# Kernel tuning notes

Measured on AMD Instinct MI355X. Metric: run time of the kernel, lower is better.

The kernel has to match this reference:

```python
import jax, jax.numpy as jnp
import numpy as np

B, S, D = 4, 2048, 1024
H, DK, DV = 16, 64, 64


def setup_inputs() -> dict:
    key = jax.random.key(0)
    ks = jax.random.split(key, 12)
    scale = 1.0 / np.sqrt(D)
    queries = jax.random.normal(ks[0], (B, S, D), dtype=jnp.float32)
    keys_ = jax.random.normal(ks[1], (B, S, D), dtype=jnp.float32)
    values = jax.random.normal(ks[2], (B, S, D), dtype=jnp.float32)
    # binary additive mask (1 = masked out), broadcastable over batch and heads
    mask = jax.random.randint(ks[3], (1, 1, S, S), 0, 2).astype(jnp.float32)
    Wq = jax.random.normal(ks[4], (D, H * DK), dtype=jnp.float32) * scale
    bq = jnp.zeros((H * DK,), dtype=jnp.float32)
    Wk = jax.random.normal(ks[5], (D, H * DK), dtype=jnp.float32) * scale
    bk = jnp.zeros((H * DK,), dtype=jnp.float32)
    Wv = jax.random.normal(ks[6], (D, H * DV), dtype=jnp.float32) * scale
    bv = jnp.zeros((H * DV,), dtype=jnp.float32)
    Wo = jax.random.normal(ks[7], (H * DV, D), dtype=jnp.float32) * scale
    bo = jnp.zeros((D,), dtype=jnp.float32)
    return {"queries": queries, "keys": keys_, "values": values, "mask": mask,
            "Wq": Wq, "bq": bq, "Wk": Wk, "bk": bk, "Wv": Wv, "bv": bv,
            "Wo": Wo, "bo": bo}


def reference(queries, keys, values, mask, Wq, bq, Wk, bk, Wv, bv, Wo, bo):
    b = queries.shape[0]
    # projections + split heads: [B, S, H*Dh] -> [B, H, S, Dh]
    q = (queries @ Wq + bq).reshape(b, -1, H, DK).transpose(0, 2, 1, 3)
    k = (keys @ Wk + bk).reshape(b, -1, H, DK).transpose(0, 2, 1, 3)
    v = (values @ Wv + bv).reshape(b, -1, H, DV).transpose(0, 2, 1, 3)
    scores = jnp.einsum("bhqd,bhkd->bhqk", q, k) / jnp.sqrt(jnp.float32(DK))
    scores = scores + mask * (-1e9)
    attn = jax.nn.softmax(scores, axis=-1)
    ctx = jnp.einsum("bhqk,bhkd->bhqd", attn, v)  # [B, H, S, DV]
    ctx = ctx.transpose(0, 2, 1, 3).reshape(b, -1, H * DV)
    return ctx @ Wo + bo
```

## Files before the change

### kernel.cpp

```cpp
#include <hip/hip_runtime.h>
#include <cstdint>
#include <cstddef>

typedef __attribute__((ext_vector_type(8))) short bf16x8;
typedef __attribute__((ext_vector_type(4))) short bf16x4;
typedef __attribute__((ext_vector_type(4))) float f32x4;

__device__ __forceinline__ unsigned short f2bf(float f) {
    union { float f; unsigned int u; } v; v.f = f;
    unsigned int r = v.u + 0x7FFFu + ((v.u >> 16) & 1u);
    return (unsigned short)(r >> 16);
}
__device__ __forceinline__ unsigned int pk2(float a, float b) {
    return (unsigned int)f2bf(a) | ((unsigned int)f2bf(b) << 16);
}
__device__ __forceinline__ unsigned int pkpair(float a, float b) {
#if __has_builtin(__builtin_amdgcn_cvt_pk_bf16_f32)
    auto r = __builtin_amdgcn_cvt_pk_bf16_f32(a, b);
    return __builtin_bit_cast(unsigned int, r);
#else
    unsigned int ua = __builtin_bit_cast(unsigned int, a) + 0x8000u;
    unsigned int ub = __builtin_bit_cast(unsigned int, b) + 0x8000u;
    return __builtin_amdgcn_perm(ub, ua, 0x07060302u);
#endif
}

typedef __attribute__((address_space(1))) void gvoid;
typedef __attribute__((address_space(3))) void svoid;
__device__ __forceinline__ void ld16_lds(const void* g, void* l) {
    __builtin_amdgcn_global_load_lds((gvoid*)g, (svoid*)l, 16, 0, 0);
}

#define QSCALE 0.1803368801111204f

__global__ __launch_bounds__(256)
void preprocess(const float* __restrict__ Qin, const float* __restrict__ Kin,
                const float* __restrict__ Vin, const float* __restrict__ Msk,
                const float* __restrict__ Wq, const float* __restrict__ Wk,
                const float* __restrict__ Wv, const float* __restrict__ Wo,
                unsigned short* __restrict__ acts, unsigned char* __restrict__ mbits,
                unsigned short* __restrict__ wts)
{
    __shared__ float t[32][33];
    const int bx = blockIdx.x, tid = threadIdx.x;
    if (bx < 12288) {
        const int which = bx >> 12;
        const float* src = (which == 0) ? Qin : (which == 1) ? Kin : Vin;
        unsigned short* dst = acts + ((size_t)which << 23);
        const size_t i = ((size_t)(bx & 4095) * 256 + tid) * 8;
        float4 a = *(const float4*)(src + i);
        float4 b = *(const float4*)(src + i + 4);
        uint4 p;
        p.x = pk2(a.x, a.y); p.y = pk2(a.z, a.w);
        p.z = pk2(b.x, b.y); p.w = pk2(b.z, b.w);
        *(uint4*)(dst + i) = p;
    } else if (bx < 14336) {
        const size_t i = ((size_t)(bx - 12288) * 256 + tid) * 8;
        float4 a = *(const float4*)(Msk + i);
        float4 b = *(const float4*)(Msk + i + 4);
        unsigned c = 0;
        c |= (a.x != 0.f) ? 1u : 0u;
        c |= (a.y != 0.f) ? 2u : 0u;
        c |= (a.z != 0.f) ? 4u : 0u;
        c |= (a.w != 0.f) ? 8u : 0u;
        c |= (b.x != 0.f) ? 16u : 0u;
        c |= (b.y != 0.f) ? 32u : 0u;
        c |= (b.z != 0.f) ? 64u : 0u;
        c |= (b.w != 0.f) ? 128u : 0u;
        mbits[i >> 3] = (unsigned char)c;
    } else {
        const int idx = bx - 14336;
        const int z = idx >> 10, rem = idx & 1023;
        const float* W = (z == 0) ? Wq : (z == 1) ? Wk : (z == 2) ? Wv : Wo;
        unsigned short* Wt = wts + ((size_t)z << 20);
        const int n0 = (rem & 31) << 5, k0 = (rem >> 5) << 5;
        const int tx = tid & 31, ty = tid >> 5;
#pragma unroll
        for (int i = 0; i < 4; i++)
            t[ty + 8 * i][tx] = W[(size_t)(k0 + ty + 8 * i) * 1024 + n0 + tx];
        __syncthreads();
#pragma unroll
        for (int i = 0; i < 4; i++)
            Wt[(size_t)(n0 + ty + 8 * i) * 1024 + k0 + tx] = f2bf(t[tx][ty + 8 * i]);
    }
}

__global__ __launch_bounds__(256, 4)
void qkv_gemm(const unsigned short* __restrict__ A0,
              const unsigned short* __restrict__ W0,
              const float* __restrict__ bq, const float* __restrict__ bk,
              const float* __restrict__ bv,
              unsigned short* __restrict__ out0)
{
    __shared__ __align__(16) unsigned short sm[18432];

    const int z = blockIdx.z;
    const unsigned short* A  = A0 + ((size_t)z << 23);
    const unsigned short* Wt = W0 + ((size_t)z << 20);
    const float* bias = (z == 0) ? bq : (z == 1) ? bk : bv;
    unsigned short* ob = out0 + ((size_t)z << 23);

    const int tid = threadIdx.x, lane = tid & 63, wave = tid >> 6;
    const int quad = lane >> 4, l16 = lane & 15;
    const int wr = wave >> 1, wc = wave & 1;
    const int m0 = blockIdx.x * 128, n0 = blockIdx.y * 128;

    const char* Ab = (const char*)A  + (size_t)m0 * 2048;
    const char* Bb = (const char*)Wt + (size_t)n0 * 2048;
    const int sr0 = tid >> 2, sc0 = (tid & 3) << 4;

    f32x4 acc[4][4];
#pragma unroll
    for (int i = 0; i < 4; i++)
#pragma unroll
        for (int j = 0; j < 4; j++) acc[i][j] = (f32x4){0.f, 0.f, 0.f, 0.f};

    {
        char* Ad = (char*)sm;
        char* Bd = Ad + 8192;
        ld16_lds(Ab + (size_t)sr0 * 2048 + sc0,        Ad + tid * 16);
        ld16_lds(Ab + (size_t)(sr0 + 64) * 2048 + sc0, Ad + (256 + tid) * 16);
        ld16_lds(Bb + (size_t)sr0 * 2048 + sc0,        Bd + tid * 16);
        ld16_lds(Bb + (size_t)(sr0 + 64) * 2048 + sc0, Bd + (256 + tid) * 16);
    }

    for (int it = 0; it < 32; ++it) {
        const int cur = it & 1;
        __syncthreads();
        if (it < 31) {
            const int kb2 = (it + 1) * 64;
            char* Ad = (char*)(sm + (cur ^ 1) * 8192);
            char* Bd = Ad + 8192;
            ld16_lds(Ab + (size_t)sr0 * 2048 + kb2 + sc0,        Ad + tid * 16);
            ld16_lds(Ab + (size_t)(sr0 + 64) * 2048 + kb2 + sc0, Ad + (256 + tid) * 16);
            ld16_lds(Bb + (size_t)sr0 * 2048 + kb2 + sc0,        Bd + tid * 16);
            ld16_lds(Bb + (size_t)(sr0 + 64) * 2048 + kb2 + sc0, Bd + (256 + tid) * 16);
        }
        const unsigned short* As = sm + cur * 8192;
        const unsigned short* Bs = As + 4096;

        bf16x8 af[4], bfr[4];
#pragma unroll
        for (int mt = 0; mt < 4; mt++)
            af[mt] = *(const bf16x8*)&As[(wr * 64 + mt * 16 + l16) * 32 + quad * 8];
#pragma unroll
        for (int nt = 0; nt < 4; nt++)
            bfr[nt] = *(const bf16x8*)&Bs[(wc * 64 + nt * 16 + l16) * 32 + quad * 8];
#pragma unroll
        for (int mt = 0; mt < 4; mt++)
#pragma unroll
            for (int nt = 0; nt < 4; nt++)
                acc[mt][nt] = __builtin_amdgcn_mfma_f32_16x16x32_bf16(af[mt], bfr[nt], acc[mt][nt], 0, 0, 0);
    }

    float bvv[4];
#pragma unroll
    for (int nt = 0; nt < 4; nt++) bvv[nt] = bias[n0 + wc * 64 + nt * 16 + l16];

    if (z < 2) {
#pragma unroll
        for (int mt = 0; mt < 4; mt++) {
            const int m = m0 + wr * 64 + mt * 16 + quad * 4;
            const int b = m >> 11;
#pragma unroll
            for (int nt = 0; nt < 4; nt++) {
                const int n = n0 + wc * 64 + nt * 16 + l16;
                const int h = n >> 6, dk = n & 63;
#pragma unroll
                for (int r = 0; r < 4; r++) {
                    const int s = (m + r) & 2047;
                    float o = acc[mt][nt][r] + bvv[nt];
                    if (z == 0) o *= QSCALE;
                    ob[((size_t)((b << 4) + h) * 2048 + s) * 64 + dk] = f2bf(o);
                }
            }
        }
    } else {
        __syncthreads();
        unsigned short* T = sm + wave * (64 * 72);
#pragma unroll
        for (int mt = 0; mt < 4; mt++)
#pragma unroll
            for (int nt = 0; nt < 4; nt++)
#pragma unroll
                for (int r = 0; r < 4; r++)
                    T[(nt * 16 + l16) * 72 + mt * 16 + quad * 4 + r] = f2bf(acc[mt][nt][r] + bvv[nt]);
        __syncthreads();
#pragma unroll
        for (int i = 0; i < 8; i++) {
            const int nl = i * 8 + (lane >> 3);
            const int mc = lane & 7;
            uint4 v = *(const uint4*)&T[nl * 72 + mc * 8];
            const int n  = n0 + wc * 64 + nl;
            const int mg = m0 + wr * 64 + mc * 8;
            const int b = mg >> 11, s = mg & 2047;
            const int h = n >> 6, dv = n & 63;
            *(uint4*)&ob[((size_t)((b << 4) + h) * 64 + dv) * 2048 + s] = v;
        }
    }
}

__global__ __launch_bounds__(256, 3)
void gemm_final(const unsigned short* __restrict__ A,
                const unsigned short* __restrict__ Wt, const float* __restrict__ bias,
                float* __restrict__ of)
{
    __shared__ __align__(16) unsigned short sm[16384];

    const int tid = threadIdx.x, lane = tid & 63, wave = tid >> 6;
    const int quad = lane >> 4, l16 = lane & 15;
    const int wr = wave >> 1, wc = wave & 1;
    const int m0 = blockIdx.x * 128, n0 = blockIdx.y * 128;

    const char* Ab = (const char*)A  + (size_t)m0 * 2048;
    const char* Bb = (const char*)Wt + (size_t)n0 * 2048;
    const int sr0 = tid >> 2, sc0 = (tid & 3) << 4;

    f32x4 acc[4][4];
#pragma unroll
    for (int i = 0; i < 4; i++)
#pragma unroll
        for (int j = 0; j < 4; j++) acc[i][j] = (f32x4){0.f, 0.f, 0.f, 0.f};

    {
        char* Ad = (char*)sm;
        char* Bd = Ad + 8192;
        ld16_lds(Ab + (size_t)sr0 * 2048 + sc0,        Ad + tid * 16);
        ld16_lds(Ab + (size_t)(sr0 + 64) * 2048 + sc0, Ad + (256 + tid) * 16);
        ld16_lds(Bb + (size_t)sr0 * 2048 + sc0,        Bd + tid * 16);
        ld16_lds(Bb + (size_t)(sr0 + 64) * 2048 + sc0, Bd + (256 + tid) * 16);
    }

    for (int it = 0; it < 32; ++it) {
        const int cur = it & 1;
        __syncthreads();
        if (it < 31) {
            const int kb2 = (it + 1) * 64;
            char* Ad = (char*)(sm + (cur ^ 1) * 8192);
            char* Bd = Ad + 8192;
            ld16_lds(Ab + (size_t)sr0 * 2048 + kb2 + sc0,        Ad + tid * 16);
            ld16_lds(Ab + (size_t)(sr0 + 64) * 2048 + kb2 + sc0, Ad + (256 + tid) * 16);
            ld16_lds(Bb + (size_t)sr0 * 2048 + kb2 + sc0,        Bd + tid * 16);
            ld16_lds(Bb + (size_t)(sr0 + 64) * 2048 + kb2 + sc0, Bd + (256 + tid) * 16);
        }
        const unsigned short* As = sm + cur * 8192;
        const unsigned short* Bs = As + 4096;

        bf16x8 af[4], bfr[4];
#pragma unroll
        for (int mt = 0; mt < 4; mt++)
            af[mt] = *(const bf16x8*)&As[(wr * 64 + mt * 16 + l16) * 32 + quad * 8];
#pragma unroll
        for (int nt = 0; nt < 4; nt++)
            bfr[nt] = *(const bf16x8*)&Bs[(wc * 64 + nt * 16 + l16) * 32 + quad * 8];
#pragma unroll
        for (int mt = 0; mt < 4; mt++)
#pragma unroll
            for (int nt = 0; nt < 4; nt++)
                acc[mt][nt] = __builtin_amdgcn_mfma_f32_16x16x32_bf16(af[mt], bfr[nt], acc[mt][nt], 0, 0, 0);
    }

    float bvv[4];
#pragma unroll
    for (int nt = 0; nt < 4; nt++) bvv[nt] = bias[n0 + wc * 64 + nt * 16 + l16];
#pragma unroll
    for (int mt = 0; mt < 4; mt++) {
        const int m = m0 + wr * 64 + mt * 16 + quad * 4;
#pragma unroll
        for (int nt = 0; nt < 4; nt++) {
            const int n = n0 + wc * 64 + nt * 16 + l16;
#pragma unroll
            for (int r = 0; r < 4; r++)
                of[(size_t)(m + r) * 1024 + n] = acc[mt][nt][r] + bvv[nt];
        }
    }
}

__global__ __launch_bounds__(256, 4)
void attn_kernel(const unsigned short* __restrict__ q,
                 const unsigned short* __restrict__ k,
                 const unsigned short* __restrict__ vT,
                 const unsigned int* __restrict__ mbits,
                 unsigned short* __restrict__ ctx)
{
    __shared__ __align__(16) unsigned short Ks[2][64 * 64];
    __shared__ __align__(16) unsigned short Vs[2][64 * 64];

    const int tid = threadIdx.x, lane = tid & 63, wave = tid >> 6;
    const int quad = lane >> 4, l16 = lane & 15;
    const int sw = l16 & 7;
    const int bid = blockIdx.x;
    const int qblk = bid & 15, h = (bid >> 4) & 15, b = bid >> 8;

    const unsigned short* qb = q  + (size_t)(b * 16 + h) * 2048 * 64;
    const unsigned short* kb = k  + (size_t)(b * 16 + h) * 2048 * 64;
    const unsigned short* vb = vT + (size_t)(b * 16 + h) * 64 * 2048;

    const int c0 = tid, c1 = 256 + tid;
    const int r0 = c0 >> 3, gcc0 = (c0 & 7) ^ (r0 & 7);
    const int r1 = c1 >> 3, gcc1 = (c1 & 7) ^ (r1 & 7);

    int qrow[2];
    bf16x8 qf[2][2];
    f32x4 O0[4], O1[4];
    f32x4 lacc0 = (f32x4){0.f,0.f,0.f,0.f}, lacc1 = (f32x4){0.f,0.f,0.f,0.f};
    const bf16x4 vones = (bf16x4){(short)0x3F80, (short)0x3F80, (short)0x3F80, (short)0x3F80};
#pragma unroll
    for (int g = 0; g < 2; g++) {
        qrow[g] = qblk * 128 + wave * 32 + g * 16 + l16;
        qf[g][0] = *(const bf16x8*)&qb[qrow[g] * 64 + quad * 8];
        qf[g][1] = *(const bf16x8*)&qb[qrow[g] * 64 + 32 + quad * 8];
    }
#pragma unroll
    for (int i = 0; i < 4; i++) { O0[i] = (f32x4){0.f,0.f,0.f,0.f}; O1[i] = (f32x4){0.f,0.f,0.f,0.f}; }
    const unsigned int* mrow0 = mbits + (size_t)qrow[0] * 64;
    const unsigned int* mrow1 = mbits + (size_t)qrow[1] * 64;

    {
        ld16_lds((const char*)kb + (size_t)r0 * 128 + gcc0 * 16, (char*)Ks[0] + c0 * 16);
        ld16_lds((const char*)kb + (size_t)r1 * 128 + gcc1 * 16, (char*)Ks[0] + c1 * 16);
        ld16_lds((const char*)vb + (size_t)r0 * 4096 + gcc0 * 16, (char*)Vs[0] + c0 * 16);
        ld16_lds((const char*)vb + (size_t)r1 * 4096 + gcc1 * 16, (char*)Vs[0] + c1 * 16);
    }
    uint2 mwc0 = *(const uint2*)&mrow0[0];
    uint2 mwc1 = *(const uint2*)&mrow1[0];

    for (int it = 0; it < 32; ++it) {
        const int kt = it << 6;
        const int cur = it & 1, nxt = cur ^ 1;
        __syncthreads();

        if (it < 31) {
            const char* kg = (const char*)kb + (size_t)(kt + 64) * 128;
            const char* vg = (const char*)vb + (size_t)(kt + 64) * 2;
            ld16_lds(kg + (size_t)r0 * 128 + gcc0 * 16, (char*)Ks[nxt] + c0 * 16);
            ld16_lds(kg + (size_t)r1 * 128 + gcc1 * 16, (char*)Ks[nxt] + c1 * 16);
            ld16_lds(vg + (size_t)r0 * 4096 + gcc0 * 16, (char*)Vs[nxt] + c0 * 16);
            ld16_lds(vg + (size_t)r1 * 4096 + gcc1 * 16, (char*)Vs[nxt] + c1 * 16);
        }
        const int mi = (it < 31) ? ((kt + 64) >> 5) : 0;
        uint2 mwn0 = *(const uint2*)&mrow0[mi];
        uint2 mwn1 = *(const uint2*)&mrow1[mi];

        const unsigned short* Kc = Ks[cur];
        const unsigned short* Vc = Vs[cur];

        f32x4 S0[4], S1[4];
        __builtin_amdgcn_s_setprio(1);
#pragma unroll
        for (int mt = 0; mt < 4; mt++) {
            const unsigned short* kp = Kc + (mt * 16 + l16) * 64;
            bf16x8 ka0 = *(const bf16x8*)&kp[((quad    ) ^ sw) * 8];
            bf16x8 ka1 = *(const bf16x8*)&kp[((4 + quad) ^ sw) * 8];
            f32x4 z0 = (f32x4){0.f,0.f,0.f,0.f};
            f32x4 z1 = (f32x4){0.f,0.f,0.f,0.f};
            z0 = __builtin_amdgcn_mfma_f32_16x16x32_bf16(ka0, qf[0][0], z0, 0, 0, 0);
            S0[mt] = __builtin_amdgcn_mfma_f32_16x16x32_bf16(ka1, qf[0][1], z0, 0, 0, 0);
            z1 = __builtin_amdgcn_mfma_f32_16x16x32_bf16(ka0, qf[1][0], z1, 0, 0, 0);
            S1[mt] = __builtin_amdgcn_mfma_f32_16x16x32_bf16(ka1, qf[1][1], z1, 0, 0, 0);
        }
        __builtin_amdgcn_s_setprio(0);
        bf16x4 pf0[4], pf1[4];
#pragma unroll
        for (int mt = 0; mt < 4; mt++) {
            const unsigned int wm0 = ((mt & 2) ? mwc0.y : mwc0.x) >> (((mt & 1) << 4) + (quad << 2));
            const unsigned int wm1 = ((mt & 2) ? mwc1.y : mwc1.x) >> (((mt & 1) << 4) + (quad << 2));
            float p0[4], p1[4];
#pragma unroll
            for (int r = 0; r < 4; r++) {
                p0[r] = __builtin_amdgcn_exp2f(((wm0 >> r) & 1u) ? -1e8f : S0[mt][r]);
                p1[r] = __builtin_amdgcn_exp2f(((wm1 >> r) & 1u) ? -1e8f : S1[mt][r]);
            }
            uint2 u0, u1;
            u0.x = pkpair(p0[0], p0[1]); u0.y = pkpair(p0[2], p0[3]);
            u1.x = pkpair(p1[0], p1[1]); u1.y = pkpair(p1[2], p1[3]);
            pf0[mt] = __builtin_bit_cast(bf16x4, u0);
            pf1[mt] = __builtin_bit_cast(bf16x4, u1);
        }
        __builtin_amdgcn_s_setprio(1);
#pragma unroll
        for (int mt = 0; mt < 4; mt++) {
            lacc0 = __builtin_amdgcn_mfma_f32_16x16x16bf16_1k(vones, pf0[mt], lacc0, 0, 0, 0);
            lacc1 = __builtin_amdgcn_mfma_f32_16x16x16bf16_1k(vones, pf1[mt], lacc1, 0, 0, 0);
        }
#pragma unroll
        for (int dvt = 0; dvt < 4; dvt++) {
            const unsigned short* vp = Vc + (dvt * 16 + l16) * 64;
#pragma unroll
            for (int mt = 0; mt < 4; mt++) {
                uint2 vv = *(const uint2*)&vp[((2 * mt + (quad >> 1)) ^ sw) * 8 + (quad & 1) * 4];
                bf16x4 va = __builtin_bit_cast(bf16x4, vv);
                O0[dvt] = __builtin_amdgcn_mfma_f32_16x16x16bf16_1k(va, pf0[mt], O0[dvt], 0, 0, 0);
                O1[dvt] = __builtin_amdgcn_mfma_f32_16x16x16bf16_1k(va, pf1[mt], O1[dvt], 0, 0, 0);
            }
        }
        __builtin_amdgcn_s_setprio(0);
        mwc0 = mwn0; mwc1 = mwn1;
    }
#pragma unroll
    for (int g = 0; g < 2; g++) {
        const float rl = __builtin_amdgcn_rcpf(g ? lacc1[0] : lacc0[0]);
        const f32x4* O = g ? O1 : O0;
#pragma unroll
        for (int dvt = 0; dvt < 4; dvt++) {
            uint2 st;
            st.x = pk2(O[dvt][0] * rl, O[dvt][1] * rl);
            st.y = pk2(O[dvt][2] * rl, O[dvt][3] * rl);
            *(uint2*)&ctx[(size_t)(b * 2048 + qrow[g]) * 1024 + h * 64 + dvt * 16 + quad * 4] = st;
        }
    }
}

extern "C" void kernel_launch(void* const* d_in, const int* in_sizes, int n_in,
                              void* d_out, int out_size, void* d_ws, size_t ws_size,
                              hipStream_t stream)
{
    const float* Qin = (const float*)d_in[0];
    const float* Kin = (const float*)d_in[1];
    const float* Vin = (const float*)d_in[2];
    const float* Msk = (const float*)d_in[3];
    const float* Wq  = (const float*)d_in[4];
    const float* bq  = (const float*)d_in[5];
    const float* Wk  = (const float*)d_in[6];
    const float* bk  = (const float*)d_in[7];
    const float* Wv  = (const float*)d_in[8];
    const float* bv  = (const float*)d_in[9];
    const float* Wo  = (const float*)d_in[10];
    const float* bo  = (const float*)d_in[11];

    unsigned short* w = (unsigned short*)d_ws;
    unsigned short* wts  = w;
    unsigned short* wto  = w + 3u * (1u << 20);
    unsigned short* qcv  = w + 4u * (1u << 20);
    unsigned short* qb   = qcv + 3u * (1u << 23);
    unsigned short* kb   = qb  + (1u << 23);
    unsigned short* vTb  = kb  + (1u << 23);
    unsigned short* ctxb = qcv;
    unsigned long long* mb = (unsigned long long*)(vTb + (1u << 23));

    preprocess<<<18432, 256, 0, stream>>>(Qin, Kin, Vin, Msk, Wq, Wk, Wv, Wo,
                                          qcv, (unsigned char*)mb, wts);
    qkv_gemm<<<dim3(64, 8, 3), 256, 0, stream>>>(qcv, wts, bq, bk, bv, qb);
    attn_kernel<<<1024, 256, 0, stream>>>(qb, kb, vTb, (const unsigned int*)mb, ctxb);
    gemm_final<<<dim3(64, 8), 256, 0, stream>>>(ctxb, wto, bo, (float*)d_out);
}
```

Measured before the change: 378.5 us.

## Software-pipeline attention loop so PV of previous tile overlaps next QK softmax

```diff
diff --git a/kernel.cpp b/kernel.cpp
--- a/kernel.cpp
+++ b/kernel.cpp
@@ -276,6 +276,68 @@
     }
 }
 
+#define ATTN_BODY(T, PFW0, PFW1, PFR0, PFR1, KC, KN, VNXT, VPREV, DOPV, DOSTAGE)   \
+{                                                                                  \
+    __syncthreads();                                                               \
+    if (DOSTAGE) {                                                                 \
+        const char* kg = (const char*)kb + (size_t)((T) + 1) * 64 * 128;           \
+        const char* vg = (const char*)vb + (size_t)((T) + 1) * 64 * 2;             \
+        ld16_lds(kg + (size_t)r0 * 128 + gcc0 * 16, (char*)(KN) + c0 * 16);        \
+        ld16_lds(kg + (size_t)r1 * 128 + gcc1 * 16, (char*)(KN) + c1 * 16);        \
+        ld16_lds(vg + (size_t)r0 * 4096 + gcc0 * 16, (char*)(VNXT) + c0 * 16);     \
+        ld16_lds(vg + (size_t)r1 * 4096 + gcc1 * 16, (char*)(VNXT) + c1 * 16);     \
+    }                                                                              \
+    const uint2 mw0 = *(const uint2*)&mrow0[(T) * 2];                              \
+    const uint2 mw1 = *(const uint2*)&mrow1[(T) * 2];                              \
+    f32x4 S0[4], S1[4];                                                            \
+    _Pragma("unroll")                                                              \
+    for (int mt = 0; mt < 4; mt++) {                                               \
+        const unsigned short* kp = (KC) + (mt * 16 + l16) * 64;                    \
+        bf16x8 ka0 = *(const bf16x8*)&kp[((quad    ) ^ sw) * 8];                   \
+        bf16x8 ka1 = *(const bf16x8*)&kp[((4 + quad) ^ sw) * 8];                   \
+        f32x4 z0 = (f32x4){0.f,0.f,0.f,0.f};                                       \
+        f32x4 z1 = (f32x4){0.f,0.f,0.f,0.f};                                       \
+        z0 = __builtin_amdgcn_mfma_f32_16x16x32_bf16(ka0, qf[0][0], z0, 0, 0, 0);  \
+        S0[mt] = __builtin_amdgcn_mfma_f32_16x16x32_bf16(ka1, qf[0][1], z0, 0, 0, 0); \
+        z1 = __builtin_amdgcn_mfma_f32_16x16x32_bf16(ka0, qf[1][0], z1, 0, 0, 0);  \
+        S1[mt] = __builtin_amdgcn_mfma_f32_16x16x32_bf16(ka1, qf[1][1], z1, 0, 0, 0); \
+    }                                                                              \
+    if (DOPV) {                                                                    \
+        _Pragma("unroll")                                                          \
+        for (int mt = 0; mt < 4; mt++) {                                           \
+            lacc0 = __builtin_amdgcn_mfma_f32_16x16x16bf16_1k(vones, PFR0[mt], lacc0, 0, 0, 0); \
+            lacc1 = __builtin_amdgcn_mfma_f32_16x16x16bf16_1k(vones, PFR1[mt], lacc1, 0, 0, 0); \
+        }                                                                          \
+        _Pragma("unroll")                                                          \
+        for (int dvt = 0; dvt < 4; dvt++) {                                        \
+            const unsigned short* vp = (VPREV) + (dvt * 16 + l16) * 64;            \
+            _Pragma("unroll")                                                      \
+            for (int mt = 0; mt < 4; mt++) {                                       \
+                uint2 vv = *(const uint2*)&vp[((2 * mt + (quad >> 1)) ^ sw) * 8 + (quad & 1) * 4]; \
+                bf16x4 va_ = __builtin_bit_cast(bf16x4, vv);                       \
+                O0[dvt] = __builtin_amdgcn_mfma_f32_16x16x16bf16_1k(va_, PFR0[mt], O0[dvt], 0, 0, 0); \
+                O1[dvt] = __builtin_amdgcn_mfma_f32_16x16x16bf16_1k(va_, PFR1[mt], O1[dvt], 0, 0, 0); \
+            }                                                                      \
+        }                                                                          \
+    }                                                                              \
+    _Pragma("unroll")                                                              \
+    for (int mt = 0; mt < 4; mt++) {                                               \
+        const unsigned int wm0 = ((mt & 2) ? mw0.y : mw0.x) >> (((mt & 1) << 4) + (quad << 2)); \
+        const unsigned int wm1 = ((mt & 2) ? mw1.y : mw1.x) >> (((mt & 1) << 4) + (quad << 2)); \
+        float p0[4], p1[4];                                                        \
+        _Pragma("unroll")                                                          \
+        for (int r = 0; r < 4; r++) {                                              \
+            p0[r] = __builtin_amdgcn_exp2f(((wm0 >> r) & 1u) ? -1e8f : S0[mt][r]); \
+            p1[r] = __builtin_amdgcn_exp2f(((wm1 >> r) & 1u) ? -1e8f : S1[mt][r]); \
+        }                                                                          \
+        uint2 u0, u1;                                                              \
+        u0.x = pkpair(p0[0], p0[1]); u0.y = pkpair(p0[2], p0[3]);                  \
+        u1.x = pkpair(p1[0], p1[1]); u1.y = pkpair(p1[2], p1[3]);                  \
+        PFW0[mt] = __builtin_bit_cast(bf16x4, u0);                                 \
+        PFW1[mt] = __builtin_bit_cast(bf16x4, u1);                                 \
+    }                                                                              \
+}
+
 __global__ __launch_bounds__(256, 4)
 void attn_kernel(const unsigned short* __restrict__ q,
                  const unsigned short* __restrict__ k,
@@ -284,7 +346,7 @@
                  unsigned short* __restrict__ ctx)
 {
     __shared__ __align__(16) unsigned short Ks[2][64 * 64];
-    __shared__ __align__(16) unsigned short Vs[2][64 * 64];
+    __shared__ __align__(16) unsigned short Vs[3][64 * 64];
 
     const int tid = threadIdx.x, lane = tid & 63, wave = tid >> 6;
     const int quad = lane >> 4, l16 = lane & 15;
@@ -322,81 +384,39 @@
         ld16_lds((const char*)vb + (size_t)r0 * 4096 + gcc0 * 16, (char*)Vs[0] + c0 * 16);
         ld16_lds((const char*)vb + (size_t)r1 * 4096 + gcc1 * 16, (char*)Vs[0] + c1 * 16);
     }
-    uint2 mwc0 = *(const uint2*)&mrow0[0];
-    uint2 mwc1 = *(const uint2*)&mrow1[0];
-
-    for (int it = 0; it < 32; ++it) {
-        const int kt = it << 6;
-        const int cur = it & 1, nxt = cur ^ 1;
-        __syncthreads();
-
-        if (it < 31) {
-            const char* kg = (const char*)kb + (size_t)(kt + 64) * 128;
-            const char* vg = (const char*)vb + (size_t)(kt + 64) * 2;
-            ld16_lds(kg + (size_t)r0 * 128 + gcc0 * 16, (char*)Ks[nxt] + c0 * 16);
-            ld16_lds(kg + (size_t)r1 * 128 + gcc1 * 16, (char*)Ks[nxt] + c1 * 16);
-            ld16_lds(vg + (size_t)r0 * 4096 + gcc0 * 16, (char*)Vs[nxt] + c0 * 16);
-            ld16_lds(vg + (size_t)r1 * 4096 + gcc1 * 16, (char*)Vs[nxt] + c1 * 16);
-        }
-        const int mi = (it < 31) ? ((kt + 64) >> 5) : 0;
-        uint2 mwn0 = *(const uint2*)&mrow0[mi];
-        uint2 mwn1 = *(const uint2*)&mrow1[mi];
-
-        const unsigned short* Kc = Ks[cur];
-        const unsigned short* Vc = Vs[cur];
-
-        f32x4 S0[4], S1[4];
-        __builtin_amdgcn_s_setprio(1);
+
+    bf16x4 pfa0[4], pfa1[4], pfb0[4], pfb1[4];
+
+    ATTN_BODY(0, pfa0, pfa1, pfb0, pfb1, Ks[0], Ks[1], Vs[1], Vs[2], false, true)
+
+    int v1 = 1;
+    for (int u = 0; u < 15; ++u) {
+        const int todd = 2 * u + 1;
+        const int s1i = (v1 == 2) ? 0 : v1 + 1;
+        const int s2i = (s1i == 2) ? 0 : s1i + 1;
+        ATTN_BODY(todd,     pfb0, pfb1, pfa0, pfa1, Ks[1], Ks[0], Vs[s1i], Vs[s2i], true, true)
+        ATTN_BODY(todd + 1, pfa0, pfa1, pfb0, pfb1, Ks[0], Ks[1], Vs[s2i], Vs[v1],  true, true)
+        v1 = s2i;
+    }
+    ATTN_BODY(31, pfb0, pfb1, pfa0, pfa1, Ks[1], Ks[0], Vs[0], Vs[0], true, false)
+
+#pragma unroll
+    for (int mt = 0; mt < 4; mt++) {
+        lacc0 = __builtin_amdgcn_mfma_f32_16x16x16bf16_1k(vones, pfb0[mt], lacc0, 0, 0, 0);
+        lacc1 = __builtin_amdgcn_mfma_f32_16x16x16bf16_1k(vones, pfb1[mt], lacc1, 0, 0, 0);
+    }
+#pragma unroll
+    for (int dvt = 0; dvt < 4; dvt++) {
+        const unsigned short* vp = Vs[1] + (dvt * 16 + l16) * 64;
 #pragma unroll
         for (int mt = 0; mt < 4; mt++) {
-            const unsigned short* kp = Kc + (mt * 16 + l16) * 64;
-            bf16x8 ka0 = *(const bf16x8*)&kp[((quad    ) ^ sw) * 8];
-            bf16x8 ka1 = *(const bf16x8*)&kp[((4 + quad) ^ sw) * 8];
-            f32x4 z0 = (f32x4){0.f,0.f,0.f,0.f};
-            f32x4 z1 = (f32x4){0.f,0.f,0.f,0.f};
-            z0 = __builtin_amdgcn_mfma_f32_16x16x32_bf16(ka0, qf[0][0], z0, 0, 0, 0);
-            S0[mt] = __builtin_amdgcn_mfma_f32_16x16x32_bf16(ka1, qf[0][1], z0, 0, 0, 0);
-            z1 = __builtin_amdgcn_mfma_f32_16x16x32_bf16(ka0, qf[1][0], z1, 0, 0, 0);
-            S1[mt] = __builtin_amdgcn_mfma_f32_16x16x32_bf16(ka1, qf[1][1], z1, 0, 0, 0);
-        }
-        __builtin_amdgcn_s_setprio(0);
-        bf16x4 pf0[4], pf1[4];
-#pragma unroll
-        for (int mt = 0; mt < 4; mt++) {
-            const unsigned int wm0 = ((mt & 2) ? mwc0.y : mwc0.x) >> (((mt & 1) << 4) + (quad << 2));
-            const unsigned int wm1 = ((mt & 2) ? mwc1.y : mwc1.x) >> (((mt & 1) << 4) + (quad << 2));
-            float p0[4], p1[4];
-#pragma unroll
-            for (int r = 0; r < 4; r++) {
-                p0[r] = __builtin_amdgcn_exp2f(((wm0 >> r) & 1u) ? -1e8f : S0[mt][r]);
-                p1[r] = __builtin_amdgcn_exp2f(((wm1 >> r) & 1u) ? -1e8f : S1[mt][r]);
-            }
-            uint2 u0, u1;
-            u0.x = pkpair(p0[0], p0[1]); u0.y = pkpair(p0[2], p0[3]);
-            u1.x = pkpair(p1[0], p1[1]); u1.y = pkpair(p1[2], p1[3]);
-            pf0[mt] = __builtin_bit_cast(bf16x4, u0);
-            pf1[mt] = __builtin_bit_cast(bf16x4, u1);
-        }
-        __builtin_amdgcn_s_setprio(1);
-#pragma unroll
-        for (int mt = 0; mt < 4; mt++) {
-            lacc0 = __builtin_amdgcn_mfma_f32_16x16x16bf16_1k(vones, pf0[mt], lacc0, 0, 0, 0);
-            lacc1 = __builtin_amdgcn_mfma_f32_16x16x16bf16_1k(vones, pf1[mt], lacc1, 0, 0, 0);
-        }
-#pragma unroll
-        for (int dvt = 0; dvt < 4; dvt++) {
-            const unsigned short* vp = Vc + (dvt * 16 + l16) * 64;
-#pragma unroll
-            for (int mt = 0; mt < 4; mt++) {
-                uint2 vv = *(const uint2*)&vp[((2 * mt + (quad >> 1)) ^ sw) * 8 + (quad & 1) * 4];
-                bf16x4 va = __builtin_bit_cast(bf16x4, vv);
-                O0[dvt] = __builtin_amdgcn_mfma_f32_16x16x16bf16_1k(va, pf0[mt], O0[dvt], 0, 0, 0);
-                O1[dvt] = __builtin_amdgcn_mfma_f32_16x16x16bf16_1k(va, pf1[mt], O1[dvt], 0, 0, 0);
-            }
-        }
-        __builtin_amdgcn_s_setprio(0);
-        mwc0 = mwn0; mwc1 = mwn1;
-    }
+            uint2 vv = *(const uint2*)&vp[((2 * mt + (quad >> 1)) ^ sw) * 8 + (quad & 1) * 4];
+            bf16x4 va_ = __builtin_bit_cast(bf16x4, vv);
+            O0[dvt] = __builtin_amdgcn_mfma_f32_16x16x16bf16_1k(va_, pfb0[mt], O0[dvt], 0, 0, 0);
+            O1[dvt] = __builtin_amdgcn_mfma_f32_16x16x16bf16_1k(va_, pfb1[mt], O1[dvt], 0, 0, 0);
+        }
+    }
+
 #pragma unroll
     for (int g = 0; g < 2; g++) {
         const float rl = __builtin_amdgcn_rcpf(g ? lacc1[0] : lacc0[0]);
```

Result: slower. 633.9 us (+67.5%).
